# Kernel tuning notes

Measured on AMD Instinct MI355X. Metric: run time of the kernel, lower is better.

The kernel has to match this reference:

```python
import jax, jax.numpy as jnp
import numpy as np

INPUT_SIZE = 1024
HIDDEN = [2048, 2048]
OUTPUT_SIZE = 10
N = 16384
PRIOR_VAR = 100.0


def setup_inputs() -> dict:
    key = jax.random.key(0)
    ks = jax.random.split(key, 8)
    X = jax.random.normal(ks[0], (N, INPUT_SIZE), dtype=jnp.float32)
    Y = jax.random.randint(ks[1], (N,), 0, OUTPUT_SIZE, dtype=jnp.int32)
    # Kaiming-ish init like nn.Linear defaults (scale irrelevant to correctness)
    def lin(k, fan_in, fan_out):
        bound = 1.0 / np.sqrt(fan_in)
        kw, kb = jax.random.split(k)
        W = jax.random.uniform(kw, (fan_out, fan_in), jnp.float32, -bound, bound)
        b = jax.random.uniform(kb, (fan_out,), jnp.float32, -bound, bound)
        return W, b
    W1, b1 = lin(ks[2], INPUT_SIZE, HIDDEN[0])
    W2, b2 = lin(ks[3], HIDDEN[0], HIDDEN[1])
    W3, b3 = lin(ks[4], HIDDEN[1], OUTPUT_SIZE)
    return {"X": X, "Y": Y, "W1": W1, "b1": b1, "W2": W2, "b2": b2, "W3": W3, "b3": b3}


def reference(X, Y, W1, b1, W2, b2, W3, b3):
    # Batched version of the per-sample Linear+ReLU+...+Linear+Softmax(dim=0) loop.
    h = jax.nn.relu(X @ W1.T + b1)            # [N, H0]
    h = jax.nn.relu(h @ W2.T + b2)            # [N, H1]
    logits = h @ W3.T + b3                    # [N, C]
    # Categorical(probs=softmax(logits)).log_prob(Y[i]) == log_softmax(logits)[i, Y[i]]
    logp = jax.nn.log_softmax(logits, axis=-1)
    log_likelihood = jnp.sum(jnp.take_along_axis(logp, Y[:, None].astype(jnp.int32), axis=-1))
    # MVN(0, 100*I) log-prob over flattened params: closed-form diagonal Gaussian.
    params = (W1, b1, W2, b2, W3, b3)
    d = sum(p.size for p in params)
    sq = sum(jnp.sum(p * p) for p in params)
    log_prior = -0.5 * (sq / PRIOR_VAR + d * jnp.log(2.0 * jnp.pi * PRIOR_VAR))
    return log_likelihood + log_prior
```

## Files before the change

kernel.cpp:

```cpp
#include <hip/hip_runtime.h>
#include <math.h>

typedef __bf16 bf16;
typedef bf16 bf16x8 __attribute__((ext_vector_type(8)));
typedef bf16 bf16x4 __attribute__((ext_vector_type(4)));
typedef float f32x4 __attribute__((ext_vector_type(4)));

#define NROWS 16384
#define HID 2048

__device__ __forceinline__ void gload_lds16(const bf16* g, bf16* l) {
  __builtin_amdgcn_global_load_lds((const __attribute__((address_space(1))) void*)g,
                                   (__attribute__((address_space(3))) void*)l,
                                   16, 0, 0);
}

#define MF(a, b, c) __builtin_amdgcn_mfma_f32_16x16x32_bf16((a), (b), (c), 0, 0, 0)

#define BAR()                                  \
  asm volatile("" ::: "memory");               \
  __builtin_amdgcn_s_barrier();                \
  asm volatile("" ::: "memory");

#define LGKM0()                                           \
  asm volatile("s_waitcnt lgkmcnt(0)" ::: "memory");      \
  __builtin_amdgcn_sched_barrier(0);

template <int K, bool RELU>
__global__ __launch_bounds__(512, 2) void gemm256(const bf16* __restrict__ A,
                                                  const bf16* __restrict__ B,
                                                  const float* __restrict__ bias,
                                                  bf16* __restrict__ C, int N) {
  extern __shared__ bf16 smem[];
  constexpr int NT = K / 32;
  const int tid = threadIdx.x;
  const int lane = tid & 63;
  const int w = tid >> 6;
  const int wr = w >> 2, wc = w & 3;

  const int xc = blockIdx.x & 7, xl = blockIdx.x >> 3;
  const int bm = xc * 8 + (xl >> 3);
  const int bn = xl & 7;

  const bf16* Abase = A + (size_t)bm * 256 * K;
  const bf16* Bbase = B + (size_t)bn * 256 * K;

  const int r0 = tid >> 2;
  const int r1 = r0 + 128;
  const int kp = tid & 3;
  const size_t offS0 = (size_t)r0 * K + ((kp ^ ((r0 >> 1) & 3)) * 8);
  const size_t offS1 = (size_t)r1 * K + ((kp ^ ((r1 >> 1) & 3)) * 8);

  int offRA[8], offRB[4];
  const int kk = lane >> 4;
#pragma unroll
  for (int mi = 0; mi < 8; ++mi) {
    const int r = wr * 128 + mi * 16 + (lane & 15);
    offRA[mi] = (r * 4 + (kk ^ ((r >> 1) & 3))) * 8;
  }
#pragma unroll
  for (int ni = 0; ni < 4; ++ni) {
    const int r = wc * 64 + ni * 16 + (lane & 15);
    offRB[ni] = (r * 4 + (kk ^ ((r >> 1) & 3))) * 8 + 8192;
  }

  f32x4 acc[8][4] = {};
  bf16x8 a0[4], a1[4], b0[4], b1[4];

#define LD8(off) (*(const bf16x8*)(smem + (off)))

#define STAGE(t, b)                                                   \
  {                                                                   \
    const bf16* As = Abase + (size_t)(t) * 32;                        \
    const bf16* Bs = Bbase + (size_t)(t) * 32;                        \
    bf16* d = smem + (b) * 16384 + w * 512;    \
    gload_lds16(As + offS0, d);                                       \
    gload_lds16(As + offS1, d + 4096);                                \
    gload_lds16(Bs + offS0, d + 8192);                                \
    gload_lds16(Bs + offS1, d + 12288);                               \
  }

#define MFMA16(AV, BV, mh)                                           \
  __builtin_amdgcn_s_setprio(1);                                     \
  acc[(mh)*4+0][0] = MF(AV[0], BV[0], acc[(mh)*4+0][0]);             \
  acc[(mh)*4+0][1] = MF(AV[0], BV[1], acc[(mh)*4+0][1]);             \
  acc[(mh)*4+0][2] = MF(AV[0], BV[2], acc[(mh)*4+0][2]);             \
  acc[(mh)*4+0][3] = MF(AV[0], BV[3], acc[(mh)*4+0][3]);             \
  acc[(mh)*4+1][0] = MF(AV[1], BV[0], acc[(mh)*4+1][0]);             \
  acc[(mh)*4+1][1] = MF(AV[1], BV[1], acc[(mh)*4+1][1]);             \
  acc[(mh)*4+1][2] = MF(AV[1], BV[2], acc[(mh)*4+1][2]);             \
  acc[(mh)*4+1][3] = MF(AV[1], BV[3], acc[(mh)*4+1][3]);             \
  acc[(mh)*4+2][0] = MF(AV[2], BV[0], acc[(mh)*4+2][0]);             \
  acc[(mh)*4+2][1] = MF(AV[2], BV[1], acc[(mh)*4+2][1]);             \
  acc[(mh)*4+2][2] = MF(AV[2], BV[2], acc[(mh)*4+2][2]);             \
  acc[(mh)*4+2][3] = MF(AV[2], BV[3], acc[(mh)*4+2][3]);             \
  acc[(mh)*4+3][0] = MF(AV[3], BV[0], acc[(mh)*4+3][0]);             \
  acc[(mh)*4+3][1] = MF(AV[3], BV[1], acc[(mh)*4+3][1]);             \
  acc[(mh)*4+3][2] = MF(AV[3], BV[2], acc[(mh)*4+3][2]);             \
  acc[(mh)*4+3][3] = MF(AV[3], BV[3], acc[(mh)*4+3][3]);             \
  __builtin_amdgcn_s_setprio(0);

  STAGE(0, 0); STAGE(1, 1); STAGE(2, 2);
  asm volatile("s_waitcnt vmcnt(8)" ::: "memory");
  BAR();
  {
#pragma unroll
    for (int i = 0; i < 4; ++i) b0[i] = LD8(offRB[i]);
#pragma unroll
    for (int i = 0; i < 4; ++i) a0[i] = LD8(offRA[i]);
  }

  for (int t = 0; t < NT; t += 2) {
    if (t + 3 < NT) STAGE(t + 3, (t + 3) & 3);
    {
      const int bb = (t & 3) * 16384;
#pragma unroll
      for (int i = 0; i < 4; ++i) a1[i] = LD8(bb + offRA[4 + i]);
    }
    MFMA16(a0, b0, 0);
    LGKM0();
    if (t + 3 < NT)      asm volatile("s_waitcnt vmcnt(8)" ::: "memory");
    else if (t + 2 < NT) asm volatile("s_waitcnt vmcnt(4)" ::: "memory");
    else                 asm volatile("s_waitcnt vmcnt(0)" ::: "memory");
    BAR();
    {
      const int nb = ((t + 1) & 3) * 16384;
#pragma unroll
      for (int i = 0; i < 4; ++i) b1[i] = LD8(nb + offRB[i]);
#pragma unroll
      for (int i = 0; i < 4; ++i) a0[i] = LD8(nb + offRA[i]);
    }
    MFMA16(a1, b0, 1);

    if (t + 4 < NT) STAGE(t + 4, (t + 4) & 3);
    {
      const int bb = ((t + 1) & 3) * 16384;
#pragma unroll
      for (int i = 0; i < 4; ++i) a1[i] = LD8(bb + offRA[4 + i]);
    }
    MFMA16(a0, b1, 0);
    LGKM0();
    if (t + 4 < NT)      asm volatile("s_waitcnt vmcnt(8)" ::: "memory");
    else if (t + 3 < NT) asm volatile("s_waitcnt vmcnt(4)" ::: "memory");
    else                 asm volatile("s_waitcnt vmcnt(0)" ::: "memory");
    if (t + 2 < NT) {
      BAR();
      const int nb = ((t + 2) & 3) * 16384;
#pragma unroll
      for (int i = 0; i < 4; ++i) b0[i] = LD8(nb + offRB[i]);
#pragma unroll
      for (int i = 0; i < 4; ++i) a0[i] = LD8(nb + offRA[i]);
    }
    MFMA16(a1, b1, 1);
  }

  const int crow0 = bm * 256 + wr * 128 + (lane >> 4) * 4;
  const int ccol0 = bn * 256 + wc * 64 + (lane & 15);
#pragma unroll
  for (int mi = 0; mi < 8; ++mi) {
#pragma unroll
    for (int ni = 0; ni < 4; ++ni) {
      const int col = ccol0 + ni * 16;
      const float bvv = bias[col];
#pragma unroll
      for (int j = 0; j < 4; ++j) {
        const int row = crow0 + mi * 16 + j;
        float v = acc[mi][ni][j] + bvv;
        if (RELU) v = fmaxf(v, 0.f);
        C[(size_t)row * N + col] = (bf16)v;
      }
    }
  }
}

struct CvtSqArgs {
  const float* src[6];
  bf16* dst[6];
  int n4[6];
  int dosq[6];
};

__global__ __launch_bounds__(256) void cvtsq_kernel(CvtSqArgs a, float* __restrict__ acc) {
  float s = 0.f;
  const int S = gridDim.x * blockDim.x;
  const int gid = blockIdx.x * blockDim.x + threadIdx.x;
#pragma unroll 1
  for (int seg = 0; seg < 6; ++seg) {
    const float4* __restrict__ src = (const float4*)a.src[seg];
    bf16x4* __restrict__ dst = (bf16x4*)a.dst[seg];
    const int n4 = a.n4[seg];
    const bool dq = a.dosq[seg] != 0;
    const int nb = n4 & ~(4 * S - 1);
    for (int i = gid; i < nb; i += 4 * S) {
      float4 v0 = src[i];
      float4 v1 = src[i + S];
      float4 v2 = src[i + 2 * S];
      float4 v3 = src[i + 3 * S];
      if (dst) {
        bf16x4 o0, o1, o2, o3;
        o0[0]=(bf16)v0.x; o0[1]=(bf16)v0.y; o0[2]=(bf16)v0.z; o0[3]=(bf16)v0.w;
        o1[0]=(bf16)v1.x; o1[1]=(bf16)v1.y; o1[2]=(bf16)v1.z; o1[3]=(bf16)v1.w;
        o2[0]=(bf16)v2.x; o2[1]=(bf16)v2.y; o2[2]=(bf16)v2.z; o2[3]=(bf16)v2.w;
        o3[0]=(bf16)v3.x; o3[1]=(bf16)v3.y; o3[2]=(bf16)v3.z; o3[3]=(bf16)v3.w;
        dst[i] = o0; dst[i + S] = o1; dst[i + 2 * S] = o2; dst[i + 3 * S] = o3;
      }
      if (dq) {
        s += v0.x*v0.x + v0.y*v0.y + v0.z*v0.z + v0.w*v0.w;
        s += v1.x*v1.x + v1.y*v1.y + v1.z*v1.z + v1.w*v1.w;
        s += v2.x*v2.x + v2.y*v2.y + v2.z*v2.z + v2.w*v2.w;
        s += v3.x*v3.x + v3.y*v3.y + v3.z*v3.z + v3.w*v3.w;
      }
    }
    for (int i = nb + gid; i < n4; i += S) {
      float4 v = src[i];
      if (dst) {
        bf16x4 o;
        o[0]=(bf16)v.x; o[1]=(bf16)v.y; o[2]=(bf16)v.z; o[3]=(bf16)v.w;
        dst[i] = o;
      }
      if (dq) s += v.x*v.x + v.y*v.y + v.z*v.z + v.w*v.w;
    }
  }
#pragma unroll
  for (int off = 32; off; off >>= 1) s += __shfl_xor(s, off, 64);
  if ((threadIdx.x & 63) == 0) atomicAdd(&acc[1], s);
}

__global__ __launch_bounds__(256) void loss_kernel(const bf16* __restrict__ h2,
                                                   const bf16* __restrict__ W3b,
                                                   const float* __restrict__ b3,
                                                   const int* __restrict__ Y,
                                                   float* __restrict__ acc) {
  __shared__ bf16 w3s[10 * HID];
  for (int i = threadIdx.x; i < 10 * HID / 8; i += 256)
    ((bf16x8*)w3s)[i] = ((const bf16x8*)W3b)[i];
  __syncthreads();

  const int lane = threadIdx.x & 63;
  const int w = threadIdx.x >> 6;
  const int nwave = gridDim.x * 4;
  float lsum = 0.f;

  for (int row = blockIdx.x * 4 + w; row < NROWS; row += nwave) {
    float p[10];
#pragma unroll
    for (int c = 0; c < 10; ++c) p[c] = 0.f;
    const bf16* hrow = h2 + (size_t)row * HID;
#pragma unroll
    for (int it = 0; it < 4; ++it) {
      const int k = it * 512 + lane * 8;
      bf16x8 hv = *(const bf16x8*)&hrow[k];
      float hf[8];
#pragma unroll
      for (int j = 0; j < 8; ++j) hf[j] = (float)hv[j];
#pragma unroll
      for (int c = 0; c < 10; ++c) {
        bf16x8 wv = *(const bf16x8*)&w3s[c * HID + k];
        float dp = 0.f;
#pragma unroll
        for (int j = 0; j < 8; ++j) dp += hf[j] * (float)wv[j];
        p[c] += dp;
      }
    }
#pragma unroll
    for (int off = 32; off; off >>= 1)
#pragma unroll
      for (int c = 0; c < 10; ++c) p[c] += __shfl_xor(p[c], off, 64);

    float lg[10], m = -1e30f;
#pragma unroll
    for (int c = 0; c < 10; ++c) { lg[c] = p[c] + b3[c]; m = fmaxf(m, lg[c]); }
    float s = 0.f;
#pragma unroll
    for (int c = 0; c < 10; ++c) s += expf(lg[c] - m);
    const float lse = m + logf(s);
    const int y = Y[row];
    float ly = 0.f;
#pragma unroll
    for (int c = 0; c < 10; ++c) ly += (c == y) ? lg[c] : 0.f;
    lsum += ly - lse;
  }
  if (lane == 0) atomicAdd(&acc[0], lsum);
}

__global__ void finalize_kernel(float* __restrict__ out, const float* __restrict__ acc,
                                const float* __restrict__ b3, double dterm) {
  double sq = (double)acc[1];
  for (int i = 0; i < 10; ++i) sq += (double)b3[i] * (double)b3[i];
  out[0] = (float)((double)acc[0] - 0.5 * (sq / 100.0 + dterm));
}

extern "C" void kernel_launch(void* const* d_in, const int* in_sizes, int n_in,
                              void* d_out, int out_size, void* d_ws, size_t ws_size,
                              hipStream_t stream) {
  const float* X  = (const float*)d_in[0];
  const int*   Y  = (const int*)d_in[1];
  const float* W1 = (const float*)d_in[2];
  const float* b1 = (const float*)d_in[3];
  const float* W2 = (const float*)d_in[4];
  const float* b2 = (const float*)d_in[5];
  const float* W3 = (const float*)d_in[6];
  const float* b3 = (const float*)d_in[7];
  float* out = (float*)d_out;

  char* ws = (char*)d_ws;
  size_t off = 0;
  auto alloc = [&](size_t bytes) -> void* {
    void* p = ws + off;
    off += (bytes + 255) & ~(size_t)255;
    return p;
  };
  bf16* Xb  = (bf16*)alloc((size_t)NROWS * 1024 * 2);
  bf16* W1b = (bf16*)alloc((size_t)HID * 1024 * 2);
  bf16* W2b = (bf16*)alloc((size_t)HID * HID * 2);
  bf16* W3b = (bf16*)alloc((size_t)10 * HID * 2);
  bf16* h1  = (bf16*)alloc((size_t)NROWS * HID * 2);
  bf16* h2  = (bf16*)alloc((size_t)NROWS * HID * 2);
  float* acc = (float*)alloc(256);

  hipMemsetAsync(acc, 0, 16, stream);

  CvtSqArgs ca;
  ca.src[0] = X;  ca.dst[0] = Xb;  ca.n4[0] = NROWS * 1024 / 4; ca.dosq[0] = 0;
  ca.src[1] = W1; ca.dst[1] = W1b; ca.n4[1] = HID * 1024 / 4;   ca.dosq[1] = 1;
  ca.src[2] = W2; ca.dst[2] = W2b; ca.n4[2] = HID * HID / 4;    ca.dosq[2] = 1;
  ca.src[3] = W3; ca.dst[3] = W3b; ca.n4[3] = 10 * HID / 4;     ca.dosq[3] = 1;
  ca.src[4] = b1; ca.dst[4] = nullptr; ca.n4[4] = HID / 4;      ca.dosq[4] = 1;
  ca.src[5] = b2; ca.dst[5] = nullptr; ca.n4[5] = HID / 4;      ca.dosq[5] = 1;
  cvtsq_kernel<<<512, 256, 0, stream>>>(ca, acc);

  hipFuncSetAttribute((const void*)gemm256<1024, true>,
                      hipFuncAttributeMaxDynamicSharedMemorySize, 131072);
  hipFuncSetAttribute((const void*)gemm256<2048, true>,
                      hipFuncAttributeMaxDynamicSharedMemorySize, 131072);

  gemm256<1024, true><<<512, 512, 131072, stream>>>(Xb, W1b, b1, h1, HID);
  gemm256<2048, true><<<512, 512, 131072, stream>>>(h1, W2b, b2, h2, HID);

  loss_kernel<<<1024, 256, 0, stream>>>(h2, W3b, b3, Y, acc);

  long long d = 0;
  for (int i = 2; i < 8; ++i) d += in_sizes[i];
  double dterm = (double)d * log(2.0 * M_PI * 100.0);
  finalize_kernel<<<1, 1, 0, stream>>>(out, acc, b3, dterm);
}
```

Before: 416.5 us.

## Add K=64 double-buffered GEMM for layer 2 and replace atomics with partial sums

Adds a second GEMM variant for the K=2048 layer. It stages 64-wide K tiles in two LDS buffers with an XOR swizzle and splits each tile's MFMAs into four quadrants, interleaved with async global-to-LDS loads. The convert/square kernel now runs on more blocks with a 2x unroll instead of 4x. The global atomics and memset are replaced by per-wave partial sums that a 256-thread finalize kernel reduces. The new GEMM's extra barriers per tile may limit overlap, and the cvtsq unroll change alters its memory-level parallelism.

Result: no change. 409.9 us (-1.6%).

```diff
diff --git a/kernel.cpp b/kernel.cpp
--- a/kernel.cpp
+++ b/kernel.cpp
@@ -27,7 +27,7 @@
   __builtin_amdgcn_sched_barrier(0);
 
 template <int K, bool RELU>
-__global__ __launch_bounds__(512, 2) void gemm256(const bf16* __restrict__ A,
+__global__ __launch_bounds__(512, 2) void gemm_r6(const bf16* __restrict__ A,
                                                   const bf16* __restrict__ B,
                                                   const float* __restrict__ bias,
                                                   bf16* __restrict__ C, int N) {
@@ -69,18 +69,18 @@
 
 #define LD8(off) (*(const bf16x8*)(smem + (off)))
 
-#define STAGE(t, b)                                                   \
+#define R6STAGE(t, b)                                                 \
   {                                                                   \
     const bf16* As = Abase + (size_t)(t) * 32;                        \
     const bf16* Bs = Bbase + (size_t)(t) * 32;                        \
-    bf16* d = smem + (b) * 16384 + w * 512;    \
+    bf16* d = smem + (b) * 16384 + w * 512;                           \
     gload_lds16(As + offS0, d);                                       \
     gload_lds16(As + offS1, d + 4096);                                \
     gload_lds16(Bs + offS0, d + 8192);                                \
     gload_lds16(Bs + offS1, d + 12288);                               \
   }
 
-#define MFMA16(AV, BV, mh)                                           \
+#define R6MFMA16(AV, BV, mh)                                         \
   __builtin_amdgcn_s_setprio(1);                                     \
   acc[(mh)*4+0][0] = MF(AV[0], BV[0], acc[(mh)*4+0][0]);             \
   acc[(mh)*4+0][1] = MF(AV[0], BV[1], acc[(mh)*4+0][1]);             \
@@ -100,7 +100,7 @@
   acc[(mh)*4+3][3] = MF(AV[3], BV[3], acc[(mh)*4+3][3]);             \
   __builtin_amdgcn_s_setprio(0);
 
-  STAGE(0, 0); STAGE(1, 1); STAGE(2, 2);
+  R6STAGE(0, 0); R6STAGE(1, 1); R6STAGE(2, 2);
   asm volatile("s_waitcnt vmcnt(8)" ::: "memory");
   BAR();
   {
@@ -111,13 +111,13 @@
   }
 
   for (int t = 0; t < NT; t += 2) {
-    if (t + 3 < NT) STAGE(t + 3, (t + 3) & 3);
+    if (t + 3 < NT) R6STAGE(t + 3, (t + 3) & 3);
     {
       const int bb = (t & 3) * 16384;
 #pragma unroll
       for (int i = 0; i < 4; ++i) a1[i] = LD8(bb + offRA[4 + i]);
     }
-    MFMA16(a0, b0, 0);
+    R6MFMA16(a0, b0, 0);
     LGKM0();
     if (t + 3 < NT)      asm volatile("s_waitcnt vmcnt(8)" ::: "memory");
     else if (t + 2 < NT) asm volatile("s_waitcnt vmcnt(4)" ::: "memory");
@@ -130,15 +130,15 @@
 #pragma unroll
       for (int i = 0; i < 4; ++i) a0[i] = LD8(nb + offRA[i]);
     }
-    MFMA16(a1, b0, 1);
-
-    if (t + 4 < NT) STAGE(t + 4, (t + 4) & 3);
+    R6MFMA16(a1, b0, 1);
+
+    if (t + 4 < NT) R6STAGE(t + 4, (t + 4) & 3);
     {
       const int bb = ((t + 1) & 3) * 16384;
 #pragma unroll
       for (int i = 0; i < 4; ++i) a1[i] = LD8(bb + offRA[4 + i]);
     }
-    MFMA16(a0, b1, 0);
+    R6MFMA16(a0, b1, 0);
     LGKM0();
     if (t + 4 < NT)      asm volatile("s_waitcnt vmcnt(8)" ::: "memory");
     else if (t + 3 < NT) asm volatile("s_waitcnt vmcnt(4)" ::: "memory");
@@ -151,7 +151,7 @@
 #pragma unroll
       for (int i = 0; i < 4; ++i) a0[i] = LD8(nb + offRA[i]);
     }
-    MFMA16(a1, b1, 1);
+    R6MFMA16(a1, b1, 1);
   }
 
   const int crow0 = bm * 256 + wr * 128 + (lane >> 4) * 4;
@@ -172,6 +172,154 @@
     }
   }
 }
+#undef R6STAGE
+#undef R6MFMA16
+
+template <int K, bool RELU>
+__global__ __launch_bounds__(512, 2) void gemm_p4(const bf16* __restrict__ A,
+                                                  const bf16* __restrict__ B,
+                                                  const float* __restrict__ bias,
+                                                  bf16* __restrict__ C, int N) {
+  extern __shared__ bf16 smem[];
+  constexpr int NT = K / 64;
+  const int tid = threadIdx.x;
+  const int lane = tid & 63;
+  const int w = tid >> 6;
+  const int wr = w >> 2, wc = w & 3;
+
+  const int xc = blockIdx.x & 7, xl = blockIdx.x >> 3;
+  const int bm = xc * 8 + (xl >> 3);
+  const int bn = xl & 7;
+
+  const bf16* Abase = A + (size_t)bm * 256 * K;
+  const bf16* Bbase = B + (size_t)bn * 256 * K;
+
+  const int srow = tid >> 3;
+  const int sslot = (tid & 7) ^ (srow & 7);
+
+  const int q0 = (lane >> 4) ^ (lane & 7);
+  const int q1 = q0 ^ 4;
+  int rA[8], rB[4];
+#pragma unroll
+  for (int mi = 0; mi < 8; ++mi)
+    rA[mi] = (wr * 128 + mi * 16 + (lane & 15)) * 64;
+#pragma unroll
+  for (int ni = 0; ni < 4; ++ni)
+    rB[ni] = 16384 + (wc * 64 + ni * 16 + (lane & 15)) * 64;
+
+  f32x4 acc[8][4] = {};
+  bf16x8 a0[8], a1[8], b0[4], b1[4];
+
+#define SOP(t, isB, h, j, bb)                                                  \
+  {                                                                            \
+    bf16* d = smem + (bb) * 32768 + (isB) * 16384 + (h) * 8192 + (j) * 4096 +  \
+              w * 512;                                                         \
+    const bf16* g = ((isB) ? Bbase : Abase) +                                  \
+                    (size_t)((h) * 128 + (j) * 64 + srow) * K +                \
+                    (size_t)(t) * 64 + sslot * 8;                              \
+    gload_lds16(g, d);                                                         \
+  }
+#define SHALF(t, isB, h, bb) SOP(t, isB, h, 0, bb) SOP(t, isB, h, 1, bb)
+
+#define QMFMA(AV, BV, mh, nh)                                                  \
+  __builtin_amdgcn_s_setprio(1);                                               \
+  acc[(mh)*4+0][(nh)*2+0] = MF(AV[0], BV[0], acc[(mh)*4+0][(nh)*2+0]);         \
+  acc[(mh)*4+0][(nh)*2+1] = MF(AV[0], BV[2], acc[(mh)*4+0][(nh)*2+1]);         \
+  acc[(mh)*4+1][(nh)*2+0] = MF(AV[2], BV[0], acc[(mh)*4+1][(nh)*2+0]);         \
+  acc[(mh)*4+1][(nh)*2+1] = MF(AV[2], BV[2], acc[(mh)*4+1][(nh)*2+1]);         \
+  acc[(mh)*4+2][(nh)*2+0] = MF(AV[4], BV[0], acc[(mh)*4+2][(nh)*2+0]);         \
+  acc[(mh)*4+2][(nh)*2+1] = MF(AV[4], BV[2], acc[(mh)*4+2][(nh)*2+1]);         \
+  acc[(mh)*4+3][(nh)*2+0] = MF(AV[6], BV[0], acc[(mh)*4+3][(nh)*2+0]);         \
+  acc[(mh)*4+3][(nh)*2+1] = MF(AV[6], BV[2], acc[(mh)*4+3][(nh)*2+1]);         \
+  acc[(mh)*4+0][(nh)*2+0] = MF(AV[1], BV[1], acc[(mh)*4+0][(nh)*2+0]);         \
+  acc[(mh)*4+0][(nh)*2+1] = MF(AV[1], BV[3], acc[(mh)*4+0][(nh)*2+1]);         \
+  acc[(mh)*4+1][(nh)*2+0] = MF(AV[3], BV[1], acc[(mh)*4+1][(nh)*2+0]);         \
+  acc[(mh)*4+1][(nh)*2+1] = MF(AV[3], BV[3], acc[(mh)*4+1][(nh)*2+1]);         \
+  acc[(mh)*4+2][(nh)*2+0] = MF(AV[5], BV[1], acc[(mh)*4+2][(nh)*2+0]);         \
+  acc[(mh)*4+2][(nh)*2+1] = MF(AV[5], BV[3], acc[(mh)*4+2][(nh)*2+1]);         \
+  acc[(mh)*4+3][(nh)*2+0] = MF(AV[7], BV[1], acc[(mh)*4+3][(nh)*2+0]);         \
+  acc[(mh)*4+3][(nh)*2+1] = MF(AV[7], BV[3], acc[(mh)*4+3][(nh)*2+1]);         \
+  __builtin_amdgcn_s_setprio(0);
+
+  SHALF(0, 0, 0, 0) SHALF(0, 0, 1, 0) SHALF(0, 1, 0, 0) SHALF(0, 1, 1, 0)
+  SHALF(1, 0, 0, 1) SHALF(1, 0, 1, 1)
+  asm volatile("s_waitcnt vmcnt(4)" ::: "memory");
+  BAR();
+
+  for (int T = 0; T < NT; ++T) {
+    const int bb = (T & 1) * 32768;
+    const int nb = 32768 - bb;
+    (void)nb;
+
+    if (T + 1 < NT) SHALF(T + 1, 1, 0, (T + 1) & 1)
+#pragma unroll
+    for (int i = 0; i < 4; ++i) {
+      a0[i * 2 + 0] = LD8(bb + rA[i] + q0 * 8);
+      a0[i * 2 + 1] = LD8(bb + rA[i] + q1 * 8);
+    }
+#pragma unroll
+    for (int i = 0; i < 2; ++i) {
+      b0[i * 2 + 0] = LD8(bb + rB[i] + q0 * 8);
+      b0[i * 2 + 1] = LD8(bb + rB[i] + q1 * 8);
+    }
+    asm volatile("s_waitcnt lgkmcnt(8)" ::: "memory");
+    BAR();
+    LGKM0();
+    QMFMA(a0, b0, 0, 0);
+    BAR();
+
+    if (T + 1 < NT) SHALF(T + 1, 1, 1, (T + 1) & 1)
+#pragma unroll
+    for (int i = 0; i < 4; ++i) {
+      a1[i * 2 + 0] = LD8(bb + rA[4 + i] + q0 * 8);
+      a1[i * 2 + 1] = LD8(bb + rA[4 + i] + q1 * 8);
+    }
+    BAR();
+    LGKM0();
+    QMFMA(a1, b0, 1, 0);
+    BAR();
+
+    if (T + 2 < NT) SHALF(T + 2, 0, 0, T & 1)
+#pragma unroll
+    for (int i = 0; i < 2; ++i) {
+      b1[i * 2 + 0] = LD8(bb + rB[2 + i] + q0 * 8);
+      b1[i * 2 + 1] = LD8(bb + rB[2 + i] + q1 * 8);
+    }
+    BAR();
+    LGKM0();
+    QMFMA(a0, b1, 0, 1);
+    BAR();
+
+    if (T + 2 < NT) SHALF(T + 2, 0, 1, T & 1)
+    QMFMA(a1, b1, 1, 1);
+    if (T + 1 < NT) {
+      if (T + 2 < NT) asm volatile("s_waitcnt vmcnt(4)" ::: "memory");
+      else            asm volatile("s_waitcnt vmcnt(0)" ::: "memory");
+      BAR();
+    }
+  }
+#undef SOP
+#undef SHALF
+#undef QMFMA
+
+  const int crow0 = bm * 256 + wr * 128 + (lane >> 4) * 4;
+  const int ccol0 = bn * 256 + wc * 64 + (lane & 15);
+#pragma unroll
+  for (int mi = 0; mi < 8; ++mi) {
+#pragma unroll
+    for (int ni = 0; ni < 4; ++ni) {
+      const int col = ccol0 + ni * 16;
+      const float bvv = bias[col];
+#pragma unroll
+      for (int j = 0; j < 4; ++j) {
+        const int row = crow0 + mi * 16 + j;
+        float v = acc[mi][ni][j] + bvv;
+        if (RELU) v = fmaxf(v, 0.f);
+        C[(size_t)row * N + col] = (bf16)v;
+      }
+    }
+  }
+}
 
 struct CvtSqArgs {
   const float* src[6];
@@ -180,7 +328,7 @@
   int dosq[6];
 };
 
-__global__ __launch_bounds__(256) void cvtsq_kernel(CvtSqArgs a, float* __restrict__ acc) {
+__global__ __launch_bounds__(256) void cvtsq_kernel(CvtSqArgs a, float* __restrict__ part) {
   float s = 0.f;
   const int S = gridDim.x * blockDim.x;
   const int gid = blockIdx.x * blockDim.x + threadIdx.x;
@@ -190,25 +338,19 @@
     bf16x4* __restrict__ dst = (bf16x4*)a.dst[seg];
     const int n4 = a.n4[seg];
     const bool dq = a.dosq[seg] != 0;
-    const int nb = n4 & ~(4 * S - 1);
-    for (int i = gid; i < nb; i += 4 * S) {
+    const int nb = n4 & ~(2 * S - 1);
+    for (int i = gid; i < nb; i += 2 * S) {
       float4 v0 = src[i];
       float4 v1 = src[i + S];
-      float4 v2 = src[i + 2 * S];
-      float4 v3 = src[i + 3 * S];
       if (dst) {
-        bf16x4 o0, o1, o2, o3;
+        bf16x4 o0, o1;
         o0[0]=(bf16)v0.x; o0[1]=(bf16)v0.y; o0[2]=(bf16)v0.z; o0[3]=(bf16)v0.w;
         o1[0]=(bf16)v1.x; o1[1]=(bf16)v1.y; o1[2]=(bf16)v1.z; o1[3]=(bf16)v1.w;
-        o2[0]=(bf16)v2.x; o2[1]=(bf16)v2.y; o2[2]=(bf16)v2.z; o2[3]=(bf16)v2.w;
-        o3[0]=(bf16)v3.x; o3[1]=(bf16)v3.y; o3[2]=(bf16)v3.z; o3[3]=(bf16)v3.w;
-        dst[i] = o0; dst[i + S] = o1; dst[i + 2 * S] = o2; dst[i + 3 * S] = o3;
+        dst[i] = o0; dst[i + S] = o1;
       }
       if (dq) {
         s += v0.x*v0.x + v0.y*v0.y + v0.z*v0.z + v0.w*v0.w;
         s += v1.x*v1.x + v1.y*v1.y + v1.z*v1.z + v1.w*v1.w;
-        s += v2.x*v2.x + v2.y*v2.y + v2.z*v2.z + v2.w*v2.w;
-        s += v3.x*v3.x + v3.y*v3.y + v3.z*v3.z + v3.w*v3.w;
       }
     }
     for (int i = nb + gid; i < n4; i += S) {
@@ -223,14 +365,14 @@
   }
 #pragma unroll
   for (int off = 32; off; off >>= 1) s += __shfl_xor(s, off, 64);
-  if ((threadIdx.x & 63) == 0) atomicAdd(&acc[1], s);
+  if ((threadIdx.x & 63) == 0) part[blockIdx.x * 4 + (threadIdx.x >> 6)] = s;
 }
 
 __global__ __launch_bounds__(256) void loss_kernel(const bf16* __restrict__ h2,
                                                    const bf16* __restrict__ W3b,
                                                    const float* __restrict__ b3,
                                                    const int* __restrict__ Y,
-                                                   float* __restrict__ acc) {
+                                                   float* __restrict__ part) {
   __shared__ bf16 w3s[10 * HID];
   for (int i = threadIdx.x; i < 10 * HID / 8; i += 256)
     ((bf16x8*)w3s)[i] = ((const bf16x8*)W3b)[i];
@@ -280,14 +422,31 @@
     for (int c = 0; c < 10; ++c) ly += (c == y) ? lg[c] : 0.f;
     lsum += ly - lse;
   }
-  if (lane == 0) atomicAdd(&acc[0], lsum);
-}
-
-__global__ void finalize_kernel(float* __restrict__ out, const float* __restrict__ acc,
-                                const float* __restrict__ b3, double dterm) {
-  double sq = (double)acc[1];
-  for (int i = 0; i < 10; ++i) sq += (double)b3[i] * (double)b3[i];
-  out[0] = (float)((double)acc[0] - 0.5 * (sq / 100.0 + dterm));
+  if (lane == 0) part[blockIdx.x * 4 + w] = lsum;
+}
+
+__global__ __launch_bounds__(256) void finalize_kernel(float* __restrict__ out,
+                                                       const float* __restrict__ part,
+                                                       const float* __restrict__ b3,
+                                                       double dterm) {
+  __shared__ float red[8];
+  float sq = 0.f, ll = 0.f;
+  for (int i = threadIdx.x; i < 8192; i += 256) sq += part[i];
+  for (int i = threadIdx.x; i < 4096; i += 256) ll += part[8192 + i];
+#pragma unroll
+  for (int off = 32; off; off >>= 1) {
+    sq += __shfl_xor(sq, off, 64);
+    ll += __shfl_xor(ll, off, 64);
+  }
+  const int w = threadIdx.x >> 6;
+  if ((threadIdx.x & 63) == 0) { red[w] = sq; red[4 + w] = ll; }
+  __syncthreads();
+  if (threadIdx.x == 0) {
+    double sqd = (double)red[0] + red[1] + red[2] + red[3];
+    double lld = (double)red[4] + red[5] + red[6] + red[7];
+    for (int i = 0; i < 10; ++i) sqd += (double)b3[i] * (double)b3[i];
+    out[0] = (float)(lld - 0.5 * (sqd / 100.0 + dterm));
+  }
 }
 
 extern "C" void kernel_launch(void* const* d_in, const int* in_sizes, int n_in,
@@ -316,9 +475,7 @@
   bf16* W3b = (bf16*)alloc((size_t)10 * HID * 2);
   bf16* h1  = (bf16*)alloc((size_t)NROWS * HID * 2);
   bf16* h2  = (bf16*)alloc((size_t)NROWS * HID * 2);
-  float* acc = (float*)alloc(256);
-
-  hipMemsetAsync(acc, 0, 16, stream);
+  float* part = (float*)alloc(12288 * 4);
 
   CvtSqArgs ca;
   ca.src[0] = X;  ca.dst[0] = Xb;  ca.n4[0] = NROWS * 1024 / 4; ca.dosq[0] = 0;
@@ -327,20 +484,20 @@
   ca.src[3] = W3; ca.dst[3] = W3b; ca.n4[3] = 10 * HID / 4;     ca.dosq[3] = 1;
   ca.src[4] = b1; ca.dst[4] = nullptr; ca.n4[4] = HID / 4;      ca.dosq[4] = 1;
   ca.src[5] = b2; ca.dst[5] = nullptr; ca.n4[5] = HID / 4;      ca.dosq[5] = 1;
-  cvtsq_kernel<<<512, 256, 0, stream>>>(ca, acc);
-
-  hipFuncSetAttribute((const void*)gemm256<1024, true>,
+  cvtsq_kernel<<<2048, 256, 0, stream>>>(ca, part);
+
+  hipFuncSetAttribute((const void*)gemm_r6<1024, true>,
                       hipFuncAttributeMaxDynamicSharedMemorySize, 131072);
-  hipFuncSetAttribute((const void*)gemm256<2048, true>,
+  hipFuncSetAttribute((const void*)gemm_p4<2048, true>,
                       hipFuncAttributeMaxDynamicSharedMemorySize, 131072);
 
-  gemm256<1024, true><<<512, 512, 131072, stream>>>(Xb, W1b, b1, h1, HID);
-  gemm256<2048, true><<<512, 512, 131072, stream>>>(h1, W2b, b2, h2, HID);
-
-  loss_kernel<<<1024, 256, 0, stream>>>(h2, W3b, b3, Y, acc);
+  gemm_r6<1024, true><<<512, 512, 131072, stream>>>(Xb, W1b, b1, h1, HID);
+  gemm_p4<2048, true><<<512, 512, 131072, stream>>>(h1, W2b, b2, h2, HID);
+
+  loss_kernel<<<1024, 256, 0, stream>>>(h2, W3b, b3, Y, part + 8192);
 
   long long d = 0;
   for (int i = 2; i < 8; ++i) d += in_sizes[i];
   double dterm = (double)d * log(2.0 * M_PI * 100.0);
-  finalize_kernel<<<1, 1, 0, stream>>>(out, acc, b3, dterm);
-}
+  finalize_kernel<<<1, 256, 0, stream>>>(out, part, b3, dterm);
+}
```
